# Kernel optimization log

Hardware: AMD Instinct MI355X
Metric: run time of the kernel (lower is better)

Reference implementation:

```python
import jax, jax.numpy as jnp
import numpy as np

D_CONV = 4
D_STATE = 16
DT_RANK = 64


def _silu(x):
    return x * jax.nn.sigmoid(x)


def setup_inputs() -> dict:
    key = jax.random.key(0)
    ks = jax.random.split(key, 10)
    B, L, dim = 2, 1024, 1024
    d_inner = 2 * dim
    s = lambda fan: 1.0 / np.sqrt(fan)
    inp = {
        "x": jax.random.normal(ks[0], (B, L, dim), jnp.float32),
        "ln_w": jnp.ones((dim,), jnp.float32),
        "ln_b": jnp.zeros((dim,), jnp.float32),
        "w_in": jax.random.normal(ks[1], (2 * d_inner, dim), jnp.float32) * s(dim),
        "conv_w": jax.random.normal(ks[2], (d_inner, D_CONV), jnp.float32) * s(D_CONV),
        "conv_b": jnp.zeros((d_inner,), jnp.float32),
        "w_xproj": jax.random.normal(ks[3], (DT_RANK + 2 * D_STATE, d_inner), jnp.float32) * s(d_inner),
        "w_dt": jax.random.normal(ks[4], (d_inner, DT_RANK), jnp.float32) * s(DT_RANK),
        "b_dt": jax.random.normal(ks[5], (d_inner,), jnp.float32) * 0.1,
        # S4D-real init: A = -(1..d_state) per channel
        "a_log": jnp.tile(jnp.log(jnp.arange(1, D_STATE + 1, dtype=jnp.float32)), (d_inner, 1)),
        "d_skip": jnp.ones((d_inner,), jnp.float32),
        "w_out": jax.random.normal(ks[6], (dim, d_inner), jnp.float32) * s(d_inner),
    }
    return inp


def reference(x, ln_w, ln_b, w_in, conv_w, conv_b, w_xproj, w_dt, b_dt, a_log, d_skip, w_out):
    B, L, dim = x.shape
    residual = x

    # LayerNorm
    mu = jnp.mean(x, axis=-1, keepdims=True)
    var = jnp.mean((x - mu) ** 2, axis=-1, keepdims=True)
    xn = (x - mu) * jax.lax.rsqrt(var + 1e-5) * ln_w + ln_b

    # in_proj -> (x_ssm, z) each (B, L, d_inner)
    xz = jnp.einsum("bld,ed->ble", xn, w_in)
    d_inner = xz.shape[-1] // 2
    xs, z = xz[..., :d_inner], xz[..., d_inner:]

    # depthwise causal conv1d (kernel D_CONV) + SiLU
    xp = jnp.pad(xs, ((0, 0), (D_CONV - 1, 0), (0, 0)))
    xc = conv_b
    for k in range(D_CONV):
        xc = xc + conv_w[:, k] * xp[:, k : k + L, :]
    u = _silu(xc)  # (B, L, d_inner)

    # x_proj -> dt, B, C
    x_dbl = jnp.einsum("ble,re->blr", u, w_xproj)
    dt_r = x_dbl[..., :DT_RANK]
    B_ssm = x_dbl[..., DT_RANK : DT_RANK + D_STATE]         # (B, L, n)
    C_ssm = x_dbl[..., DT_RANK + D_STATE :]                 # (B, L, n)

    dt = jax.nn.softplus(jnp.einsum("blr,er->ble", dt_r, w_dt) + b_dt)  # (B, L, d_inner)

    A = -jnp.exp(a_log)  # (d_inner, n)
    deltaA = jnp.exp(jnp.einsum("ble,en->blen", dt, A))            # (B, L, e, n)
    deltaBu = jnp.einsum("ble,bln,ble->blen", dt, B_ssm, u)        # (B, L, e, n)

    # selective scan over L
    def step(h, ins):
        dA_t, dBu_t, C_t = ins
        h = dA_t * h + dBu_t                       # (B, e, n)
        y = jnp.einsum("ben,bn->be", h, C_t)
        return h, y

    h0 = jnp.zeros((B, d_inner, D_STATE), xs.dtype)
    _, ys = jax.lax.scan(
        step,
        h0,
        (deltaA.transpose(1, 0, 2, 3), deltaBu.transpose(1, 0, 2, 3), C_ssm.transpose(1, 0, 2)),
    )
    y = ys.transpose(1, 0, 2) + u * d_skip         # (B, L, e)

    y = y * _silu(z)
    out = jnp.einsum("ble,de->bld", y, w_out)
    return residual + out
```

## Files before the change

kernel.cpp:

```cpp
#include <hip/hip_runtime.h>
#include <hip/hip_bf16.h>


#define LC 32
#define NCHUNK 32

typedef short bf16x8 __attribute__((ext_vector_type(8)));
typedef float f32x4  __attribute__((ext_vector_type(4)));

static __device__ __forceinline__ float siluf(float x) { return x / (1.f + __expf(-x)); }
static __device__ __forceinline__ unsigned short f2bf(float f) {
    unsigned int u = __float_as_uint(f);
    unsigned int r = (u + 0x7fffu + ((u >> 16) & 1u)) >> 16;
    return (unsigned short)r;
}
static __device__ __forceinline__ void gload_lds16(const void* g, void* l) {
    __builtin_amdgcn_global_load_lds(
        (const __attribute__((address_space(1))) void*)g,
        (__attribute__((address_space(3))) void*)l, 16, 0, 0);
}

__global__ __launch_bounds__(256) void f2b_dual(
    const float* __restrict__ in0, unsigned short* __restrict__ out0, int n0,
    const float* __restrict__ in1, unsigned short* __restrict__ out1, int n1)
{
    int i = blockIdx.x * 256 + threadIdx.x;
    if (i < n0) {
        float4 v = reinterpret_cast<const float4*>(in0)[i];
        ushort4 o = { f2bf(v.x), f2bf(v.y), f2bf(v.z), f2bf(v.w) };
        reinterpret_cast<ushort4*>(out0)[i] = o;
    } else if (i - n0 < n1) {
        int j = i - n0;
        float4 v = reinterpret_cast<const float4*>(in1)[j];
        ushort4 o = { f2bf(v.x), f2bf(v.y), f2bf(v.z), f2bf(v.w) };
        reinterpret_cast<ushort4*>(out1)[j] = o;
    }
}

__global__ __launch_bounds__(256) void f2b_kernel(
    const float* __restrict__ in, unsigned short* __restrict__ out, int n4)
{
    int i = blockIdx.x * 256 + threadIdx.x;
    if (i < n4) {
        float4 v = reinterpret_cast<const float4*>(in)[i];
        ushort4 o = { f2bf(v.x), f2bf(v.y), f2bf(v.z), f2bf(v.w) };
        reinterpret_cast<ushort4*>(out)[i] = o;
    }
}

__global__ __launch_bounds__(256) void ln_kernel(
    const float* __restrict__ x,
    const float* __restrict__ w,
    const float* __restrict__ bias,
    unsigned short* __restrict__ xn)
{
    int m = blockIdx.x, tid = threadIdx.x;
    const float4* xr = reinterpret_cast<const float4*>(x) + (size_t)m * 256;
    float4 r = xr[tid];
    float f0 = r.x, f1 = r.y, f2 = r.z, f3 = r.w;
    float s  = f0 + f1 + f2 + f3;
    float s2 = f0*f0 + f1*f1 + f2*f2 + f3*f3;
    #pragma unroll
    for (int off = 32; off > 0; off >>= 1) {
        s  += __shfl_down(s, off);
        s2 += __shfl_down(s2, off);
    }
    __shared__ float red[8];
    if ((tid & 63) == 0) { red[tid >> 6] = s; red[4 + (tid >> 6)] = s2; }
    __syncthreads();
    float st = red[0] + red[1] + red[2] + red[3];
    float qt = red[4] + red[5] + red[6] + red[7];
    float mu   = st * (1.f / 1024.f);
    float var  = qt * (1.f / 1024.f) - mu * mu;
    float rstd = rsqrtf(var + 1e-5f);
    float4 wv = reinterpret_cast<const float4*>(w)[tid];
    float4 bv = reinterpret_cast<const float4*>(bias)[tid];
    ushort4 o = { f2bf((f0 - mu) * rstd * wv.x + bv.x),
                  f2bf((f1 - mu) * rstd * wv.y + bv.y),
                  f2bf((f2 - mu) * rstd * wv.z + bv.z),
                  f2bf((f3 - mu) * rstd * wv.w + bv.w) };
    reinterpret_cast<ushort4*>(xn + (size_t)m * 1024)[tid] = o;
}

__global__ __launch_bounds__(256) void gemm_bf16_nt(
    const unsigned short* __restrict__ A, int lda,
    const unsigned short* __restrict__ B, int ldb,
    int Kslice,
    float* __restrict__ C, int ldc,
    const float* __restrict__ bias,
    const float* __restrict__ resid,
    int ep, size_t Cstride)
{
    __shared__ short As[128 * 32];
    __shared__ short Bs[64 * 32];
    int tid = threadIdx.x;
    int z = blockIdx.z;
    A += (size_t)z * Kslice;
    B += (size_t)z * Kslice;
    C += (size_t)z * Cstride;
    int m0 = blockIdx.y * 128, n0 = blockIdx.x * 64;
    int lane = tid & 63, wave = tid >> 6;
    int wm = (wave >> 1) * 64, wn = (wave & 1) * 32;
    int frow = lane & 15, fq = lane >> 4;

    f32x4 acc[4][2] = {};

    int lrow = lane >> 2;
    int scol = (lane & 3) * 8;
    const unsigned short* AgL = A + (size_t)(m0 + wave * 32 + lrow) * lda + scol;
    const unsigned short* BgL = B + (size_t)(n0 + wave * 16 + lrow) * ldb + scol;
    short* AsW = As + (wave * 32) * 32;
    short* BsW = Bs + (wave * 16) * 32;

    for (int k0 = 0; k0 < Kslice; k0 += 32) {
        __syncthreads();
        gload_lds16(AgL + k0,                     AsW);
        gload_lds16(AgL + (size_t)16 * lda + k0,  AsW + 16 * 32);
        gload_lds16(BgL + k0,                     BsW);
        __syncthreads();
        bf16x8 af[4], bfr[2];
        #pragma unroll
        for (int i = 0; i < 4; ++i)
            af[i] = *reinterpret_cast<const bf16x8*>(As + (wm + i * 16 + frow) * 32 + fq * 8);
        #pragma unroll
        for (int j = 0; j < 2; ++j)
            bfr[j] = *reinterpret_cast<const bf16x8*>(Bs + (wn + j * 16 + frow) * 32 + fq * 8);
        #pragma unroll
        for (int i = 0; i < 4; ++i)
            #pragma unroll
            for (int j = 0; j < 2; ++j)
                acc[i][j] = __builtin_amdgcn_mfma_f32_16x16x32_bf16(af[i], bfr[j], acc[i][j], 0, 0, 0);
    }

    int cn = lane & 15, rq = (lane >> 4) * 4;
    #pragma unroll
    for (int i = 0; i < 4; ++i) {
        #pragma unroll
        for (int j = 0; j < 2; ++j) {
            #pragma unroll
            for (int r = 0; r < 4; ++r) {
                int row = m0 + wm + i * 16 + rq + r;
                int col = n0 + wn + j * 16 + cn;
                float v = acc[i][j][r];
                if (ep == 0) {
                    C[(size_t)row * ldc + col] = v;
                } else if (ep == 1) {
                    v += bias[col];
                    v = (v > 20.f) ? v : log1pf(__expf(v));
                    C[(size_t)row * ldc + col] = v;
                } else {
                    v += resid[(size_t)row * ldc + col];
                    C[(size_t)row * ldc + col] = v;
                }
            }
        }
    }
}

__global__ __launch_bounds__(256) void out_reduce(
    const float* __restrict__ part, const float* __restrict__ x,
    float* __restrict__ out)
{
    int i = blockIdx.x * 256 + threadIdx.x;
    float4 s = reinterpret_cast<const float4*>(x)[i];
    #pragma unroll
    for (int z = 0; z < 4; ++z) {
        float4 p = reinterpret_cast<const float4*>(part + (size_t)z * 2097152)[i];
        s.x += p.x; s.y += p.y; s.z += p.z; s.w += p.w;
    }
    reinterpret_cast<float4*>(out)[i] = s;
}

__global__ __launch_bounds__(256) void xproj_splitk(
    const float* __restrict__ A,
    const float* __restrict__ B,
    float* __restrict__ part)
{
    __shared__ float As[16][68];
    __shared__ float Bs[16][100];
    int tid = threadIdx.x;
    int m0 = blockIdx.x * 64;
    int k0 = blockIdx.y * 128;
    int tx = tid & 15;
    int ty = tid >> 4;
    float acc[4][6] = {};
    int arow = tid >> 2, akg = (tid & 3) << 2;
    int brow1 = (256 + tid) >> 2, bkg1 = ((256 + tid) & 3) << 2;

    for (int ks = 0; ks < 128; ks += 16) {
        float4 av = *reinterpret_cast<const float4*>(A + (size_t)(m0 + arow) * 2048 + k0 + ks + akg);
        float4 bv0 = make_float4(0.f, 0.f, 0.f, 0.f), bv1 = bv0;
        if (arow < 96)  bv0 = *reinterpret_cast<const float4*>(B + (size_t)arow * 2048 + k0 + ks + akg);
        if (brow1 < 96) bv1 = *reinterpret_cast<const float4*>(B + (size_t)brow1 * 2048 + k0 + ks + bkg1);
        __syncthreads();
        As[akg + 0][arow] = av.x; As[akg + 1][arow] = av.y;
        As[akg + 2][arow] = av.z; As[akg + 3][arow] = av.w;
        if (arow < 96) {
            Bs[akg + 0][arow] = bv0.x; Bs[akg + 1][arow] = bv0.y;
            Bs[akg + 2][arow] = bv0.z; Bs[akg + 3][arow] = bv0.w;
        }
        if (brow1 < 96) {
            Bs[bkg1 + 0][brow1] = bv1.x; Bs[bkg1 + 1][brow1] = bv1.y;
            Bs[bkg1 + 2][brow1] = bv1.z; Bs[bkg1 + 3][brow1] = bv1.w;
        }
        __syncthreads();
        #pragma unroll
        for (int k = 0; k < 16; ++k) {
            float aa[4], bb[6];
            #pragma unroll
            for (int i = 0; i < 4; ++i) aa[i] = As[k][ty * 4 + i];
            #pragma unroll
            for (int j = 0; j < 6; ++j) bb[j] = Bs[k][tx * 6 + j];
            #pragma unroll
            for (int i = 0; i < 4; ++i)
                #pragma unroll
                for (int j = 0; j < 6; ++j)
                    acc[i][j] = fmaf(aa[i], bb[j], acc[i][j]);
        }
    }
    float* p = part + (size_t)blockIdx.y * 196608;
    #pragma unroll
    for (int i = 0; i < 4; ++i)
        #pragma unroll
        for (int j = 0; j < 6; ++j)
            p[(size_t)(m0 + ty * 4 + i) * 96 + tx * 6 + j] = acc[i][j];
}

__global__ __launch_bounds__(256) void xproj_reduce(
    const float* __restrict__ part, float* __restrict__ xdbl,
    unsigned short* __restrict__ dtr)
{
    int i = blockIdx.x * 256 + threadIdx.x;
    float s = 0.f;
    #pragma unroll
    for (int sd = 0; sd < 16; ++sd) s += part[(size_t)sd * 196608 + i];
    xdbl[i] = s;
    int m = i / 96, col = i - m * 96;
    if (col < 64) dtr[(size_t)m * 64 + col] = f2bf(s);
}

__global__ __launch_bounds__(256) void conv_silu_kernel(
    const float* __restrict__ xz,
    const float* __restrict__ cw,
    const float* __restrict__ cb,
    float* __restrict__ u)
{
    int idx = blockIdx.x * 256 + threadIdx.x;
    int e = idx & 2047;
    int m = idx >> 11;
    int l = m & 1023;
    float acc = cb[e];
    #pragma unroll
    for (int k = 0; k < 4; ++k) {
        int ls = l - 3 + k;
        if (ls >= 0)
            acc += cw[e * 4 + k] * xz[(size_t)(m - 3 + k) * 4096 + e];
    }
    u[(size_t)m * 2048 + e] = siluf(acc);
}

__global__ __launch_bounds__(256) void scan_part1(
    const float* __restrict__ dt,
    const float* __restrict__ u,
    const float* __restrict__ xdbl,
    const float* __restrict__ a_log,
    float* __restrict__ hpart,
    float* __restrict__ Aprod)
{
    int tid = threadIdx.x;
    int ch = tid >> 2, ng = tid & 3;
    int bid = blockIdx.x;
    int c = bid & 31, et = (bid >> 5) & 31, b = bid >> 10;
    int e = et * 64 + ch;
    float4 al = *reinterpret_cast<const float4*>(a_log + e * 16 + ng * 4);
    float A0 = -__expf(al.x), A1 = -__expf(al.y), A2 = -__expf(al.z), A3 = -__expf(al.w);
    size_t rbase = (size_t)b * 1024 + c * LC;
    const float* dt_p = dt + rbase * 2048 + e;
    const float* u_p  = u  + rbase * 2048 + e;
    const float* b_p  = xdbl + rbase * 96 + 64 + ng * 4;
    float h0 = 0.f, h1 = 0.f, h2 = 0.f, h3 = 0.f;
    float P0 = 1.f, P1 = 1.f, P2 = 1.f, P3 = 1.f;
    #pragma unroll 4
    for (int l = 0; l < LC; ++l) {
        float dt_v = dt_p[(size_t)l * 2048];
        float u_v  = u_p[(size_t)l * 2048];
        float4 Bv  = *reinterpret_cast<const float4*>(b_p + (size_t)l * 96);
        float du = dt_v * u_v;
        float d0 = __expf(dt_v * A0), d1 = __expf(dt_v * A1);
        float d2 = __expf(dt_v * A2), d3 = __expf(dt_v * A3);
        h0 = fmaf(d0, h0, du * Bv.x); P0 *= d0;
        h1 = fmaf(d1, h1, du * Bv.y); P1 *= d1;
        h2 = fmaf(d2, h2, du * Bv.z); P2 *= d2;
        h3 = fmaf(d3, h3, du * Bv.w); P3 *= d3;
    }
    size_t oidx = (size_t)c * 65536 + ((size_t)b * 2048 + e) * 16 + ng * 4;
    *reinterpret_cast<float4*>(hpart + oidx) = make_float4(h0, h1, h2, h3);
    *reinterpret_cast<float4*>(Aprod + oidx) = make_float4(P0, P1, P2, P3);
}

__global__ __launch_bounds__(256) void scan_combine(
    const float* __restrict__ hpart,
    const float* __restrict__ Aprod,
    float* __restrict__ hinit)
{
    int t = (blockIdx.x * 256 + threadIdx.x) * 4;
    float4 h = make_float4(0.f, 0.f, 0.f, 0.f);
    #pragma unroll
    for (int c = 0; c < NCHUNK; ++c) {
        *reinterpret_cast<float4*>(hinit + (size_t)c * 65536 + t) = h;
        float4 P = *reinterpret_cast<const float4*>(Aprod + (size_t)c * 65536 + t);
        float4 hp = *reinterpret_cast<const float4*>(hpart + (size_t)c * 65536 + t);
        h.x = fmaf(P.x, h.x, hp.x);
        h.y = fmaf(P.y, h.y, hp.y);
        h.z = fmaf(P.z, h.z, hp.z);
        h.w = fmaf(P.w, h.w, hp.w);
    }
}

__global__ __launch_bounds__(256) void scan_part2(
    const float* __restrict__ dt,
    const float* __restrict__ u,
    const float* __restrict__ xdbl,
    const float* __restrict__ xz,
    const float* __restrict__ a_log,
    const float* __restrict__ d_skip,
    const float* __restrict__ hinit,
    unsigned short* __restrict__ y)
{
    int tid = threadIdx.x;
    int ch = tid >> 2, ng = tid & 3;
    int bid = blockIdx.x;
    int c = bid & 31, et = (bid >> 5) & 31, b = bid >> 10;
    int e = et * 64 + ch;
    float4 al = *reinterpret_cast<const float4*>(a_log + e * 16 + ng * 4);
    float A0 = -__expf(al.x), A1 = -__expf(al.y), A2 = -__expf(al.z), A3 = -__expf(al.w);
    float dsk = d_skip[e];
    size_t rbase = (size_t)b * 1024 + c * LC;
    const float* dt_p = dt + rbase * 2048 + e;
    const float* u_p  = u  + rbase * 2048 + e;
    const float* z_p  = xz + rbase * 4096 + 2048 + e;
    const float* bc_p = xdbl + rbase * 96 + 64 + ng * 4;
    unsigned short* y_p = y + rbase * 2048 + e;
    size_t oidx = (size_t)c * 65536 + ((size_t)b * 2048 + e) * 16 + ng * 4;
    float4 hi = *reinterpret_cast<const float4*>(hinit + oidx);
    float h0 = hi.x, h1 = hi.y, h2 = hi.z, h3 = hi.w;
    #pragma unroll 4
    for (int l = 0; l < LC; ++l) {
        float dt_v = dt_p[(size_t)l * 2048];
        float u_v  = u_p[(size_t)l * 2048];
        float4 Bv  = *reinterpret_cast<const float4*>(bc_p + (size_t)l * 96);
        float4 Cv  = *reinterpret_cast<const float4*>(bc_p + (size_t)l * 96 + 16);
        float du = dt_v * u_v;
        float d0 = __expf(dt_v * A0), d1 = __expf(dt_v * A1);
        float d2 = __expf(dt_v * A2), d3 = __expf(dt_v * A3);
        h0 = fmaf(d0, h0, du * Bv.x);
        h1 = fmaf(d1, h1, du * Bv.y);
        h2 = fmaf(d2, h2, du * Bv.z);
        h3 = fmaf(d3, h3, du * Bv.w);
        float p = h0 * Cv.x + h1 * Cv.y + h2 * Cv.z + h3 * Cv.w;
        p += __shfl_xor(p, 1);
        p += __shfl_xor(p, 2);
        if (ng == 0) {
            float zv = z_p[(size_t)l * 4096];
            y_p[(size_t)l * 2048] = f2bf((p + u_v * dsk) * siluf(zv));
        }
    }
}

extern "C" void kernel_launch(void* const* d_in, const int* in_sizes, int n_in,
                              void* d_out, int out_size, void* d_ws, size_t ws_size,
                              hipStream_t stream) {
    const float* x       = (const float*)d_in[0];
    const float* ln_w    = (const float*)d_in[1];
    const float* ln_b    = (const float*)d_in[2];
    const float* w_in    = (const float*)d_in[3];
    const float* conv_w  = (const float*)d_in[4];
    const float* conv_b  = (const float*)d_in[5];
    const float* w_xproj = (const float*)d_in[6];
    const float* w_dt    = (const float*)d_in[7];
    const float* b_dt    = (const float*)d_in[8];
    const float* a_log   = (const float*)d_in[9];
    const float* d_skip  = (const float*)d_in[10];
    const float* w_out   = (const float*)d_in[11];
    float* out = (float*)d_out;

    float* ws = (float*)d_ws;
    unsigned short* xn_b    = (unsigned short*)(ws);
    float* xz    = ws + 1048576;
    float* u     = ws + 9437184;
    float* xdbl  = ws + 13631488;
    float* dt    = ws + 13828096;
    float* hpart = ws + 18022400;
    float* Aprod = ws + 20119552;
    float* hinit = ws + 22216704;
    float* xpart = ws + 18022400;
    float* opart = xz;
    unsigned short* y_b     = (unsigned short*)(ws + 18022400);
    unsigned short* w_in_b  = (unsigned short*)(ws + 21168128);
    unsigned short* w_out_b = (unsigned short*)(ws + 23265280);
    unsigned short* w_dt_b  = (unsigned short*)(ws + 24313856);
    unsigned short* dtr_b   = (unsigned short*)(ws + 24379392);

    f2b_dual<<<4224, 256, 0, stream>>>(w_in, w_in_b, 1048576, w_dt, w_dt_b, 32768);
    ln_kernel<<<2048, 256, 0, stream>>>(x, ln_w, ln_b, xn_b);
    gemm_bf16_nt<<<dim3(64, 16, 1), 256, 0, stream>>>(xn_b, 1024, w_in_b, 1024, 1024,
                                                      xz, 4096, nullptr, nullptr, 0, 0);
    conv_silu_kernel<<<16384, 256, 0, stream>>>(xz, conv_w, conv_b, u);
    xproj_splitk<<<dim3(32, 16), 256, 0, stream>>>(u, w_xproj, xpart);
    xproj_reduce<<<768, 256, 0, stream>>>(xpart, xdbl, dtr_b);
    gemm_bf16_nt<<<dim3(32, 16, 1), 256, 0, stream>>>(dtr_b, 64, w_dt_b, 64, 64,
                                                      dt, 2048, b_dt, nullptr, 1, 0);
    scan_part1<<<2048, 256, 0, stream>>>(dt, u, xdbl, a_log, hpart, Aprod);
    scan_combine<<<64, 256, 0, stream>>>(hpart, Aprod, hinit);
    scan_part2<<<2048, 256, 0, stream>>>(dt, u, xdbl, xz, a_log, d_skip, hinit, y_b);
    f2b_kernel<<<2048, 256, 0, stream>>>(w_out, w_out_b, 524288);
    gemm_bf16_nt<<<dim3(16, 16, 4), 256, 0, stream>>>(y_b, 2048, w_out_b, 2048, 512,
                                                      opart, 1024, nullptr, nullptr, 0, 2097152);
    out_reduce<<<2048, 256, 0, stream>>>(opart, x, out);
}
```

Measured before the change: 285.4 us.

## Double-buffer GEMM LDS tiles, prefetch scan inputs, merge weight conversions

```diff
diff --git a/kernel.cpp b/kernel.cpp
--- a/kernel.cpp
+++ b/kernel.cpp
@@ -20,32 +20,20 @@
         (__attribute__((address_space(3))) void*)l, 16, 0, 0);
 }
 
-__global__ __launch_bounds__(256) void f2b_dual(
-    const float* __restrict__ in0, unsigned short* __restrict__ out0, int n0,
-    const float* __restrict__ in1, unsigned short* __restrict__ out1, int n1)
+__global__ __launch_bounds__(256) void f2b_all(
+    const float* __restrict__ w_in,  unsigned short* __restrict__ w_in_b,
+    const float* __restrict__ w_out, unsigned short* __restrict__ w_out_b,
+    const float* __restrict__ w_dt,  unsigned short* __restrict__ w_dt_b)
 {
     int i = blockIdx.x * 256 + threadIdx.x;
-    if (i < n0) {
-        float4 v = reinterpret_cast<const float4*>(in0)[i];
-        ushort4 o = { f2bf(v.x), f2bf(v.y), f2bf(v.z), f2bf(v.w) };
-        reinterpret_cast<ushort4*>(out0)[i] = o;
-    } else if (i - n0 < n1) {
-        int j = i - n0;
-        float4 v = reinterpret_cast<const float4*>(in1)[j];
-        ushort4 o = { f2bf(v.x), f2bf(v.y), f2bf(v.z), f2bf(v.w) };
-        reinterpret_cast<ushort4*>(out1)[j] = o;
-    }
-}
-
-__global__ __launch_bounds__(256) void f2b_kernel(
-    const float* __restrict__ in, unsigned short* __restrict__ out, int n4)
-{
-    int i = blockIdx.x * 256 + threadIdx.x;
-    if (i < n4) {
-        float4 v = reinterpret_cast<const float4*>(in)[i];
-        ushort4 o = { f2bf(v.x), f2bf(v.y), f2bf(v.z), f2bf(v.w) };
-        reinterpret_cast<ushort4*>(out)[i] = o;
-    }
+    const float* in; unsigned short* outp; int j;
+    if (i < 1048576)      { in = w_in;  outp = w_in_b;  j = i; }
+    else if (i < 1572864) { in = w_out; outp = w_out_b; j = i - 1048576; }
+    else if (i < 1605632) { in = w_dt;  outp = w_dt_b;  j = i - 1572864; }
+    else return;
+    float4 v = reinterpret_cast<const float4*>(in)[j];
+    ushort4 o = { f2bf(v.x), f2bf(v.y), f2bf(v.z), f2bf(v.w) };
+    reinterpret_cast<ushort4*>(outp)[j] = o;
 }
 
 __global__ __launch_bounds__(256) void ln_kernel(
@@ -91,8 +79,8 @@
     const float* __restrict__ resid,
     int ep, size_t Cstride)
 {
-    __shared__ short As[128 * 32];
-    __shared__ short Bs[64 * 32];
+    __shared__ short As[2 * 128 * 32];
+    __shared__ short Bs[2 * 64 * 32];
     int tid = threadIdx.x;
     int z = blockIdx.z;
     A += (size_t)z * Kslice;
@@ -109,27 +97,38 @@
     int scol = (lane & 3) * 8;
     const unsigned short* AgL = A + (size_t)(m0 + wave * 32 + lrow) * lda + scol;
     const unsigned short* BgL = B + (size_t)(n0 + wave * 16 + lrow) * ldb + scol;
-    short* AsW = As + (wave * 32) * 32;
-    short* BsW = Bs + (wave * 16) * 32;
-
+    int aoff = (wave * 32) * 32;
+    int boff = (wave * 16) * 32;
+
+    gload_lds16(AgL,                      As + aoff);
+    gload_lds16(AgL + (size_t)16 * lda,   As + aoff + 16 * 32);
+    gload_lds16(BgL,                      Bs + boff);
+
+    int cur = 0;
     for (int k0 = 0; k0 < Kslice; k0 += 32) {
         __syncthreads();
-        gload_lds16(AgL + k0,                     AsW);
-        gload_lds16(AgL + (size_t)16 * lda + k0,  AsW + 16 * 32);
-        gload_lds16(BgL + k0,                     BsW);
-        __syncthreads();
+        int nk = k0 + 32;
+        if (nk < Kslice) {
+            int nxt = cur ^ 1;
+            gload_lds16(AgL + nk,                     As + nxt * 4096 + aoff);
+            gload_lds16(AgL + (size_t)16 * lda + nk,  As + nxt * 4096 + aoff + 16 * 32);
+            gload_lds16(BgL + nk,                     Bs + nxt * 2048 + boff);
+        }
+        const short* Ac = As + cur * 4096;
+        const short* Bc = Bs + cur * 2048;
         bf16x8 af[4], bfr[2];
         #pragma unroll
         for (int i = 0; i < 4; ++i)
-            af[i] = *reinterpret_cast<const bf16x8*>(As + (wm + i * 16 + frow) * 32 + fq * 8);
+            af[i] = *reinterpret_cast<const bf16x8*>(Ac + (wm + i * 16 + frow) * 32 + fq * 8);
         #pragma unroll
         for (int j = 0; j < 2; ++j)
-            bfr[j] = *reinterpret_cast<const bf16x8*>(Bs + (wn + j * 16 + frow) * 32 + fq * 8);
+            bfr[j] = *reinterpret_cast<const bf16x8*>(Bc + (wn + j * 16 + frow) * 32 + fq * 8);
         #pragma unroll
         for (int i = 0; i < 4; ++i)
             #pragma unroll
             for (int j = 0; j < 2; ++j)
                 acc[i][j] = __builtin_amdgcn_mfma_f32_16x16x32_bf16(af[i], bfr[j], acc[i][j], 0, 0, 0);
+        cur ^= 1;
     }
 
     int cn = lane & 15, rq = (lane >> 4) * 4;
@@ -280,18 +279,22 @@
     const float* b_p  = xdbl + rbase * 96 + 64 + ng * 4;
     float h0 = 0.f, h1 = 0.f, h2 = 0.f, h3 = 0.f;
     float P0 = 1.f, P1 = 1.f, P2 = 1.f, P3 = 1.f;
+    float dt_c = dt_p[0];
+    float u_c  = u_p[0];
+    float4 B_c = *reinterpret_cast<const float4*>(b_p);
     #pragma unroll 4
     for (int l = 0; l < LC; ++l) {
-        float dt_v = dt_p[(size_t)l * 2048];
-        float u_v  = u_p[(size_t)l * 2048];
-        float4 Bv  = *reinterpret_cast<const float4*>(b_p + (size_t)l * 96);
-        float du = dt_v * u_v;
-        float d0 = __expf(dt_v * A0), d1 = __expf(dt_v * A1);
-        float d2 = __expf(dt_v * A2), d3 = __expf(dt_v * A3);
-        h0 = fmaf(d0, h0, du * Bv.x); P0 *= d0;
-        h1 = fmaf(d1, h1, du * Bv.y); P1 *= d1;
-        h2 = fmaf(d2, h2, du * Bv.z); P2 *= d2;
-        h3 = fmaf(d3, h3, du * Bv.w); P3 *= d3;
+        float dt_n = dt_p[(size_t)(l + 1) * 2048];
+        float u_n  = u_p[(size_t)(l + 1) * 2048];
+        float4 B_n = *reinterpret_cast<const float4*>(b_p + (size_t)(l + 1) * 96);
+        float du = dt_c * u_c;
+        float d0 = __expf(dt_c * A0), d1 = __expf(dt_c * A1);
+        float d2 = __expf(dt_c * A2), d3 = __expf(dt_c * A3);
+        h0 = fmaf(d0, h0, du * B_c.x); P0 *= d0;
+        h1 = fmaf(d1, h1, du * B_c.y); P1 *= d1;
+        h2 = fmaf(d2, h2, du * B_c.z); P2 *= d2;
+        h3 = fmaf(d3, h3, du * B_c.w); P3 *= d3;
+        dt_c = dt_n; u_c = u_n; B_c = B_n;
     }
     size_t oidx = (size_t)c * 65536 + ((size_t)b * 2048 + e) * 16 + ng * 4;
     *reinterpret_cast<float4*>(hpart + oidx) = make_float4(h0, h1, h2, h3);
@@ -344,26 +347,31 @@
     size_t oidx = (size_t)c * 65536 + ((size_t)b * 2048 + e) * 16 + ng * 4;
     float4 hi = *reinterpret_cast<const float4*>(hinit + oidx);
     float h0 = hi.x, h1 = hi.y, h2 = hi.z, h3 = hi.w;
+    float dt_c = dt_p[0];
+    float u_c  = u_p[0];
+    float4 B_c = *reinterpret_cast<const float4*>(bc_p);
+    float4 C_c = *reinterpret_cast<const float4*>(bc_p + 16);
     #pragma unroll 4
     for (int l = 0; l < LC; ++l) {
-        float dt_v = dt_p[(size_t)l * 2048];
-        float u_v  = u_p[(size_t)l * 2048];
-        float4 Bv  = *reinterpret_cast<const float4*>(bc_p + (size_t)l * 96);
-        float4 Cv  = *reinterpret_cast<const float4*>(bc_p + (size_t)l * 96 + 16);
-        float du = dt_v * u_v;
-        float d0 = __expf(dt_v * A0), d1 = __expf(dt_v * A1);
-        float d2 = __expf(dt_v * A2), d3 = __expf(dt_v * A3);
-        h0 = fmaf(d0, h0, du * Bv.x);
-        h1 = fmaf(d1, h1, du * Bv.y);
-        h2 = fmaf(d2, h2, du * Bv.z);
-        h3 = fmaf(d3, h3, du * Bv.w);
-        float p = h0 * Cv.x + h1 * Cv.y + h2 * Cv.z + h3 * Cv.w;
+        float dt_n = dt_p[(size_t)(l + 1) * 2048];
+        float u_n  = u_p[(size_t)(l + 1) * 2048];
+        float4 B_n = *reinterpret_cast<const float4*>(bc_p + (size_t)(l + 1) * 96);
+        float4 C_n = *reinterpret_cast<const float4*>(bc_p + (size_t)(l + 1) * 96 + 16);
+        float du = dt_c * u_c;
+        float d0 = __expf(dt_c * A0), d1 = __expf(dt_c * A1);
+        float d2 = __expf(dt_c * A2), d3 = __expf(dt_c * A3);
+        h0 = fmaf(d0, h0, du * B_c.x);
+        h1 = fmaf(d1, h1, du * B_c.y);
+        h2 = fmaf(d2, h2, du * B_c.z);
+        h3 = fmaf(d3, h3, du * B_c.w);
+        float p = h0 * C_c.x + h1 * C_c.y + h2 * C_c.z + h3 * C_c.w;
         p += __shfl_xor(p, 1);
         p += __shfl_xor(p, 2);
         if (ng == 0) {
             float zv = z_p[(size_t)l * 4096];
-            y_p[(size_t)l * 2048] = f2bf((p + u_v * dsk) * siluf(zv));
-        }
+            y_p[(size_t)l * 2048] = f2bf((p + u_c * dsk) * siluf(zv));
+        }
+        dt_c = dt_n; u_c = u_n; B_c = B_n; C_c = C_n;
     }
 }
 
@@ -397,11 +405,11 @@
     float* opart = xz;
     unsigned short* y_b     = (unsigned short*)(ws + 18022400);
     unsigned short* w_in_b  = (unsigned short*)(ws + 21168128);
-    unsigned short* w_out_b = (unsigned short*)(ws + 23265280);
     unsigned short* w_dt_b  = (unsigned short*)(ws + 24313856);
     unsigned short* dtr_b   = (unsigned short*)(ws + 24379392);
-
-    f2b_dual<<<4224, 256, 0, stream>>>(w_in, w_in_b, 1048576, w_dt, w_dt_b, 32768);
+    unsigned short* w_out_b = (unsigned short*)(ws + 24444928);
+
+    f2b_all<<<6272, 256, 0, stream>>>(w_in, w_in_b, w_out, w_out_b, w_dt, w_dt_b);
     ln_kernel<<<2048, 256, 0, stream>>>(x, ln_w, ln_b, xn_b);
     gemm_bf16_nt<<<dim3(64, 16, 1), 256, 0, stream>>>(xn_b, 1024, w_in_b, 1024, 1024,
                                                       xz, 4096, nullptr, nullptr, 0, 0);
@@ -413,7 +421,6 @@
     scan_part1<<<2048, 256, 0, stream>>>(dt, u, xdbl, a_log, hpart, Aprod);
     scan_combine<<<64, 256, 0, stream>>>(hpart, Aprod, hinit);
     scan_part2<<<2048, 256, 0, stream>>>(dt, u, xdbl, xz, a_log, d_skip, hinit, y_b);
-    f2b_kernel<<<2048, 256, 0, stream>>>(w_out, w_out_b, 524288);
     gemm_bf16_nt<<<dim3(16, 16, 4), 256, 0, stream>>>(y_b, 2048, w_out_b, 2048, 512,
                                                       opart, 1024, nullptr, nullptr, 0, 2097152);
     out_reduce<<<2048, 256, 0, stream>>>(opart, x, out);
```

New measurement: 279.6 us. -2.0%, faster.
